# Kernel optimization log

Measured on AMD Instinct MI355X. Metric: run time of the kernel, lower is better.

The kernel has to match this reference:

```python
import jax, jax.numpy as jnp
import numpy as np

# OGB feature vocab sizes
ATOM_DIMS = [119, 4, 12, 12, 10, 6, 6, 2, 2]
BOND_DIMS = [5, 6, 2]
ATOM_OFF = np.concatenate([[0], np.cumsum(ATOM_DIMS)[:-1]]).astype(np.int32)
BOND_OFF = np.concatenate([[0], np.cumsum(BOND_DIMS)[:-1]]).astype(np.int32)
SCHEDULE_LEN = 5   # len(train_schedule) == len(eval_schedule)
NUM_GRAPHS = 12000
BN_EPS = 1e-5

N_NODES, N_EDGES, HIDDEN, NUM_TASKS = 300000, 600000, 128, 128


def setup_inputs() -> dict:
    key = jax.random.key(0)
    ks = jax.random.split(key, 16)
    x = jax.random.randint(ks[0], (N_NODES, 9), 0, 2, dtype=jnp.int32)
    edge_index = jax.random.randint(ks[1], (2, N_EDGES), 0, N_NODES, dtype=jnp.int32)
    edge_attr = jax.random.randint(ks[2], (N_EDGES, 3), 0, 2, dtype=jnp.int32)
    batch = jnp.sort(jax.random.randint(ks[3], (N_NODES,), 0, NUM_GRAPHS, dtype=jnp.int32))
    # learned parameters (embedding tables concatenated with offsets)
    atom_emb = jax.random.normal(ks[4], (sum(ATOM_DIMS), HIDDEN), jnp.float32) * 0.1
    bond_emb = jax.random.normal(ks[5], (sum(BOND_DIMS), HIDDEN), jnp.float32) * 0.1
    conv_W = jax.random.normal(ks[6], (HIDDEN, HIDDEN), jnp.float32) * (1.0 / np.sqrt(HIDDEN))
    conv_b = jnp.zeros((HIDDEN,), jnp.float32)
    root_emb = jax.random.normal(ks[7], (HIDDEN,), jnp.float32) * 0.1
    bn_gamma = jnp.ones((HIDDEN,), jnp.float32)
    bn_beta = jnp.zeros((HIDDEN,), jnp.float32)
    bn_mean = jnp.zeros((HIDDEN,), jnp.float32)   # running stats (eval mode)
    bn_var = jnp.ones((HIDDEN,), jnp.float32)
    lin_W = jax.random.normal(ks[8], (NUM_TASKS, HIDDEN), jnp.float32) * (1.0 / np.sqrt(HIDDEN))
    lin_b = jnp.zeros((NUM_TASKS,), jnp.float32)
    return {"x": x, "edge_index": edge_index, "edge_attr": edge_attr, "batch": batch,
            "atom_emb": atom_emb, "bond_emb": bond_emb, "conv_W": conv_W, "conv_b": conv_b,
            "root_emb": root_emb, "bn_gamma": bn_gamma, "bn_beta": bn_beta,
            "bn_mean": bn_mean, "bn_var": bn_var, "lin_W": lin_W, "lin_b": lin_b}


def reference(x, edge_index, edge_attr, batch, atom_emb, bond_emb, conv_W, conv_b,
              root_emb, bn_gamma, bn_beta, bn_mean, bn_var, lin_W, lin_b):
    N = x.shape[0]
    # AtomEncoder / BondEncoder: sum of per-feature embedding lookups
    h = atom_emb[x + jnp.asarray(ATOM_OFF, x.dtype)].sum(axis=1)            # [N, H]
    e = bond_emb[edge_attr + jnp.asarray(BOND_OFF, edge_attr.dtype)].sum(axis=1)  # [E, H]
    row, col = edge_index[0], edge_index[1]
    deg = jax.ops.segment_sum(jnp.ones_like(row, h.dtype), row, num_segments=N) + 1.0  # [N]
    dis = deg ** -0.5                                                        # deg >= 1, no inf
    norm = dis[row] * dis[col]                                               # [E]
    inv_std = bn_gamma / jnp.sqrt(bn_var + BN_EPS)
    for i in range(SCHEDULE_LEN):
        old = h
        z = h @ conv_W.T + conv_b                                            # [N, H]
        # message: norm * relu(x_j + edge_emb), aggregated at target (col) via scatter-add
        msg = norm[:, None] * jax.nn.relu(z[row] + e)                        # [E, H]
        agg = jax.ops.segment_sum(msg, col, num_segments=N)                  # [N, H]
        z = agg + jax.nn.relu(z + root_emb) / deg[:, None]                   # self-loop term
        z = jax.nn.relu(z)
        z = (z - bn_mean) * inv_std + bn_beta                                # BN (eval, running stats)
        # dropout: identity in eval mode
        # NOTE: faithful to source bug: smooth_fac is the loop index i, not schedule[i]
        h = i * old + (1 - i) * z
    # global mean pool over graphs
    counts = jax.ops.segment_sum(jnp.ones((N,), h.dtype), batch, num_segments=NUM_GRAPHS)
    pooled = jax.ops.segment_sum(h, batch, num_segments=NUM_GRAPHS) / jnp.maximum(counts, 1.0)[:, None]
    return pooled @ lin_W.T + lin_b                                          # [num_graphs, num_tasks]
```

## Files before the change

### kernel.cpp

```cpp
#include <hip/hip_runtime.h>

#define HID 128
#define AROWS 173

__device__ __forceinline__ int lcol(int p) { return ((p & 7) << 4) | (p >> 3); }

typedef __attribute__((ext_vector_type(8))) short short8;
typedef __attribute__((ext_vector_type(8))) unsigned short ushort8v;
typedef __attribute__((ext_vector_type(4))) float floatx4;
typedef __attribute__((ext_vector_type(4))) unsigned short ushort4v;

__device__ __forceinline__ unsigned short f2bf(float f) {
    unsigned u = __builtin_bit_cast(unsigned, f);
    u += 0x7FFF + ((u >> 16) & 1);
    return (unsigned short)(u >> 16);
}
__device__ __forceinline__ float bf2f(unsigned short s) {
    unsigned u = ((unsigned)s) << 16;
    return __builtin_bit_cast(float, u);
}

__global__ void fillrd_kernel(float* __restrict__ dis, int* __restrict__ indeg, int N)
{
    int i = blockIdx.x * 256 + threadIdx.x;
    if (i < N) { dis[i] = 0.f; indeg[i] = 0; }
}

__global__ void diag_kernel(float* __restrict__ out, long n, float val)
{
    long i = (long)blockIdx.x * blockDim.x + threadIdx.x;
    if (i < n) out[i] = val;
}

__global__ __launch_bounds__(256) void tables_kernel(
    const float* __restrict__ conv_W, unsigned short* __restrict__ Wb,
    const float* __restrict__ lin_W, unsigned short* __restrict__ linWb,
    const float* __restrict__ bond_emb, unsigned short* __restrict__ comb,
    const float* __restrict__ gamma, const float* __restrict__ beta,
    const float* __restrict__ mean, const float* __restrict__ var,
    float* __restrict__ bnsc, float* __restrict__ bnsh,
    const float* __restrict__ root, const float* __restrict__ conv_b,
    float* __restrict__ rootp, float* __restrict__ cbp)
{
    int blk = blockIdx.x;
    int tid = threadIdx.x;
    if (blk < 64) {
        int i = blk * 256 + tid;
        int row = i >> 7, p = i & 127;
        Wb[i] = f2bf(conv_W[row * HID + lcol(p)]);
    } else if (blk < 128) {
        int i = (blk - 64) * 256 + tid;
        int row = i >> 7, p = i & 127;
        linWb[i] = f2bf(lin_W[row * HID + lcol(p)]);
    } else if (blk < 158) {
        int i = (blk - 128) * 2 + (tid >> 7);
        int p = tid & 127;
        int c = lcol(p);
        int a0 = i / 12, a1 = (i % 12) / 2, a2 = i % 2;
        comb[i * HID + p] = f2bf(bond_emb[a0 * HID + c] + bond_emb[(5 + a1) * HID + c]
                               + bond_emb[(11 + a2) * HID + c]);
    } else if (tid < HID) {
        int c = lcol(tid);
        float sc = gamma[c] * rsqrtf(var[c] + 1e-5f);
        bnsc[tid] = sc;
        bnsh[tid] = beta[c] - mean[c] * sc;
        rootp[tid] = root[c];
        cbp[tid] = conv_b[c];
    }
}

__global__ __launch_bounds__(128) void ewk_kernel(
    const float* __restrict__ atom_emb, const float* __restrict__ conv_W,
    unsigned short* __restrict__ EWb)
{
    int r = blockIdx.x;
    int c = threadIdx.x;
    const float* er = atom_emb + (long)r * HID;
    const float* wr = conv_W + (long)c * HID;
    float acc = 0.f;
#pragma unroll 4
    for (int k = 0; k < HID; k += 4) {
        floatx4 e4 = *reinterpret_cast<const floatx4*>(er + k);
        floatx4 w4 = *reinterpret_cast<const floatx4*>(wr + k);
        acc += e4[0] * w4[0] + e4[1] * w4[1] + e4[2] * w4[2] + e4[3] * w4[3];
    }
    EWb[(long)r * HID + ((c & 15) * 8 + (c >> 4))] = f2bf(acc);
}

__global__ void hist_kernel(const int* __restrict__ ei, float* __restrict__ dis,
                            int* __restrict__ indeg, int E)
{
    for (int e = blockIdx.x * blockDim.x + threadIdx.x; e < E; e += gridDim.x * blockDim.x) {
        atomicAdd(&dis[ei[e]], 1.f);
        atomicAdd(&indeg[ei[E + e]], 1);
    }
}

__global__ __launch_bounds__(256) void bsum_kernel(
    const int* __restrict__ indeg, int* __restrict__ partial,
    float* __restrict__ dis, int N)
{
    __shared__ int s[256];
    int tid = threadIdx.x;
    int i = blockIdx.x * 256 + tid;
    int v = (i < N) ? indeg[i] : 0;
    s[tid] = v;
    if (i < N) dis[i] = rsqrtf(dis[i] + 1.f);
    __syncthreads();
    for (int d = 128; d > 0; d >>= 1) {
        if (tid < d) s[tid] += s[tid + d];
        __syncthreads();
    }
    if (tid == 0) partial[blockIdx.x] = s[0];
}

__global__ __launch_bounds__(256) void scan1_kernel(
    const int* __restrict__ partial, int* __restrict__ offs,
    int* __restrict__ ptr, int B, int N)
{
    __shared__ int s[256];
    __shared__ int carry_s;
    int tid = threadIdx.x;
    if (tid == 0) carry_s = 0;
    __syncthreads();
    for (int base = 0; base < B; base += 256) {
        int i = base + tid;
        int v = (i < B) ? partial[i] : 0;
        s[tid] = v;
        __syncthreads();
        for (int d = 1; d < 256; d <<= 1) {
            int t = (tid >= d) ? s[tid - d] : 0;
            __syncthreads();
            s[tid] += t;
            __syncthreads();
        }
        int carry = carry_s;
        if (i < B) offs[i] = carry + s[tid] - v;
        __syncthreads();
        if (tid == 0) carry_s = carry + s[255];
        __syncthreads();
    }
    if (tid == 0) ptr[N] = carry_s;
}

__global__ __launch_bounds__(256) void scan2_kernel(
    const int* __restrict__ indeg, const int* __restrict__ offs,
    int* __restrict__ ptr, int* __restrict__ cursor, int N)
{
    __shared__ int s[256];
    int tid = threadIdx.x;
    int i = blockIdx.x * 256 + tid;
    int v = (i < N) ? indeg[i] : 0;
    s[tid] = v;
    __syncthreads();
    for (int d = 1; d < 256; d <<= 1) {
        int t = (tid >= d) ? s[tid - d] : 0;
        __syncthreads();
        s[tid] += t;
        __syncthreads();
    }
    if (i < N) {
        int ex = offs[blockIdx.x] + s[tid] - v;
        ptr[i] = ex;
        cursor[i] = ex;
    }
}

__global__ void fillcsr_kernel(const int* __restrict__ ei, const int* __restrict__ attr,
                               const float* __restrict__ dis, int* __restrict__ cursor,
                               int2* __restrict__ edata, const int* __restrict__ batch,
                               int* __restrict__ gptr, int E, int N, int G)
{
    for (int e = blockIdx.x * blockDim.x + threadIdx.x; e < E; e += gridDim.x * blockDim.x) {
        int r   = ei[e];
        int col = ei[E + e];
        int pos = atomicAdd(&cursor[col], 1);
        int ci  = attr[e * 3] * 12 + attr[e * 3 + 1] * 2 + attr[e * 3 + 2];
        float nrm = dis[r] * dis[col];
        int2 ed;
        ed.x = r;
        ed.y = ci | ((int)f2bf(nrm) << 16);
        edata[pos] = ed;
    }
    for (int n = blockIdx.x * blockDim.x + threadIdx.x; n < N; n += gridDim.x * blockDim.x) {
        int b = batch[n];
        int bp = (n == 0) ? -1 : batch[n - 1];
        for (int g = bp + 1; g <= b; ++g) gptr[g] = n;
        if (n == N - 1)
            for (int g = b + 1; g <= G; ++g) gptr[g] = N;
    }
}

__global__ __launch_bounds__(256) void enc_kernel(
    const int* __restrict__ x, const unsigned short* __restrict__ EWb,
    const float* __restrict__ cbp, unsigned short* __restrict__ zb, int N)
{
    long n = (long)blockIdx.x * 16 + (threadIdx.x >> 4);
    if (n >= N) return;
    int c = (threadIdx.x & 15) * 8;
    const int OFF[9] = {0, 119, 123, 135, 147, 157, 163, 169, 171};

    float acc[8];
#pragma unroll
    for (int j = 0; j < 8; ++j) acc[j] = cbp[c + j];

#pragma unroll
    for (int f = 0; f < 9; ++f) {
        int idx = x[n * 9 + f] + OFF[f];
        ushort8v v = *reinterpret_cast<const ushort8v*>(EWb + (long)idx * HID + c);
#pragma unroll
        for (int j = 0; j < 8; ++j) acc[j] += bf2f(v[j]);
    }

    ushort8v o;
#pragma unroll
    for (int j = 0; j < 8; ++j) o[j] = f2bf(acc[j]);
    *reinterpret_cast<ushort8v*>(zb + n * HID + c) = o;
}

template<bool FIRST>
__global__ __launch_bounds__(256) void agg_kernel(
    const int* __restrict__ ptr, const int2* __restrict__ edata,
    const unsigned short* __restrict__ comb, const float* __restrict__ dis,
    const float* __restrict__ root, const float* __restrict__ bnsc,
    const float* __restrict__ bnsh, const unsigned short* __restrict__ zb,
    unsigned short* __restrict__ hb, float fi, int N)
{
    long n = (long)blockIdx.x * 16 + (threadIdx.x >> 4);
    if (n >= N) return;
    int c = (threadIdx.x & 15) * 8;

    ushort8v zv = *reinterpret_cast<const ushort8v*>(zb + n * HID + c);
    ushort8v hv;
    if constexpr (!FIRST) hv = *reinterpret_cast<const ushort8v*>(hb + n * HID + c);
    float di = dis[n];
    float rd = di * di;
    float acc[8];
#pragma unroll
    for (int j = 0; j < 8; ++j) acc[j] = fmaxf(bf2f(zv[j]) + root[c + j], 0.f) * rd;

    int jb = ptr[n], je = ptr[n + 1];
    int j2 = jb;
    for (; j2 + 1 < je; j2 += 2) {
        int2 e0 = edata[j2];
        int2 e1 = edata[j2 + 1];
        ushort8v z0 = *reinterpret_cast<const ushort8v*>(zb + (long)e0.x * HID + c);
        ushort8v z1 = *reinterpret_cast<const ushort8v*>(zb + (long)e1.x * HID + c);
        ushort8v c0 = *reinterpret_cast<const ushort8v*>(comb + (e0.y & 0xFF) * HID + c);
        ushort8v c1 = *reinterpret_cast<const ushort8v*>(comb + (e1.y & 0xFF) * HID + c);
        float n0 = bf2f((unsigned short)(((unsigned)e0.y) >> 16));
        float n1 = bf2f((unsigned short)(((unsigned)e1.y) >> 16));
#pragma unroll
        for (int j = 0; j < 8; ++j) {
            acc[j] += fmaxf(bf2f(z0[j]) + bf2f(c0[j]), 0.f) * n0;
            acc[j] += fmaxf(bf2f(z1[j]) + bf2f(c1[j]), 0.f) * n1;
        }
    }
    if (j2 < je) {
        int2 e0 = edata[j2];
        ushort8v z0 = *reinterpret_cast<const ushort8v*>(zb + (long)e0.x * HID + c);
        ushort8v c0 = *reinterpret_cast<const ushort8v*>(comb + (e0.y & 0xFF) * HID + c);
        float n0 = bf2f((unsigned short)(((unsigned)e0.y) >> 16));
#pragma unroll
        for (int j = 0; j < 8; ++j)
            acc[j] += fmaxf(bf2f(z0[j]) + bf2f(c0[j]), 0.f) * n0;
    }

    ushort8v o;
#pragma unroll
    for (int j = 0; j < 8; ++j) {
        float t = fmaxf(acc[j], 0.f) * bnsc[c + j] + bnsh[c + j];
        float h;
        if constexpr (FIRST) h = t;
        else h = fi * bf2f(hv[j]) + (1.f - fi) * t;
        o[j] = f2bf(h);
    }
    *reinterpret_cast<ushort8v*>(hb + n * HID + c) = o;
}

__global__ void gemm_kernel(
    const unsigned short* __restrict__ hb, const unsigned short* __restrict__ Wb,
    const float* __restrict__ bias, unsigned short* __restrict__ zb, int N)
{
    int tid = threadIdx.x;
    int wave = tid >> 6;
    int lane = tid & 63;
    int l15 = lane & 15;
    int q = lane >> 4;
    long row0 = (long)blockIdx.x * 128 + wave * 32;

    short8 a[2][4];
#pragma unroll
    for (int mt = 0; mt < 2; ++mt) {
        long rl = row0 + mt * 16 + l15;
        if (rl > (long)N - 1) rl = (long)N - 1;
        const unsigned short* ap = hb + rl * HID + q * 8;
#pragma unroll
        for (int kb = 0; kb < 4; ++kb)
            a[mt][kb] = *reinterpret_cast<const short8*>(ap + kb * 32);
    }

    floatx4 acc[2][8];
#pragma unroll
    for (int mt = 0; mt < 2; ++mt)
#pragma unroll
        for (int nt = 0; nt < 8; ++nt) {
            floatx4 zz = {0.f, 0.f, 0.f, 0.f};
            acc[mt][nt] = zz;
        }

#pragma unroll
    for (int nt = 0; nt < 8; ++nt) {
        const unsigned short* bp = Wb + (nt * 16 + l15) * HID + q * 8;
#pragma unroll
        for (int kb = 0; kb < 4; ++kb) {
            short8 b = *reinterpret_cast<const short8*>(bp + kb * 32);
            acc[0][nt] = __builtin_amdgcn_mfma_f32_16x16x32_bf16(a[0][kb], b, acc[0][nt], 0, 0, 0);
            acc[1][nt] = __builtin_amdgcn_mfma_f32_16x16x32_bf16(a[1][kb], b, acc[1][nt], 0, 0, 0);
        }
    }

    float bi[8];
#pragma unroll
    for (int nt = 0; nt < 8; ++nt) bi[nt] = bias[nt * 16 + l15];

#pragma unroll
    for (int mt = 0; mt < 2; ++mt)
#pragma unroll
        for (int r = 0; r < 4; ++r) {
            long gr = row0 + mt * 16 + q * 4 + r;
            if (gr < N) {
                ushort8v o;
#pragma unroll
                for (int nt = 0; nt < 8; ++nt)
                    o[nt] = f2bf(acc[mt][nt][r] + bi[nt]);
                *reinterpret_cast<ushort8v*>(zb + gr * HID + l15 * 8) = o;
            }
        }
}

__global__ __launch_bounds__(256) void linmm_kernel(
    const unsigned short* __restrict__ pb, const unsigned short* __restrict__ Wb,
    const float* __restrict__ bias, float* __restrict__ out, int G)
{
    int wave = threadIdx.x >> 6;
    int lane = threadIdx.x & 63;
    int l15 = lane & 15;
    int q = lane >> 4;
    long row0 = (long)blockIdx.x * 128 + wave * 32;

    short8 a[2][4];
#pragma unroll
    for (int mt = 0; mt < 2; ++mt) {
        long rl = row0 + mt * 16 + l15;
        if (rl > (long)G - 1) rl = (long)G - 1;
        const unsigned short* ap = pb + rl * HID + q * 8;
#pragma unroll
        for (int kb = 0; kb < 4; ++kb)
            a[mt][kb] = *reinterpret_cast<const short8*>(ap + kb * 32);
    }

    floatx4 acc[2][8];
#pragma unroll
    for (int mt = 0; mt < 2; ++mt)
#pragma unroll
        for (int nt = 0; nt < 8; ++nt) {
            floatx4 zz = {0.f, 0.f, 0.f, 0.f};
            acc[mt][nt] = zz;
        }

#pragma unroll
    for (int nt = 0; nt < 8; ++nt) {
        const unsigned short* bp = Wb + (nt * 16 + l15) * HID + q * 8;
#pragma unroll
        for (int kb = 0; kb < 4; ++kb) {
            short8 b = *reinterpret_cast<const short8*>(bp + kb * 32);
            acc[0][nt] = __builtin_amdgcn_mfma_f32_16x16x32_bf16(a[0][kb], b, acc[0][nt], 0, 0, 0);
            acc[1][nt] = __builtin_amdgcn_mfma_f32_16x16x32_bf16(a[1][kb], b, acc[1][nt], 0, 0, 0);
        }
    }

    float bi[8];
#pragma unroll
    for (int nt = 0; nt < 8; ++nt) bi[nt] = bias[nt * 16 + l15];

#pragma unroll
    for (int mt = 0; mt < 2; ++mt)
#pragma unroll
        for (int r = 0; r < 4; ++r) {
            long rr = row0 + mt * 16 + q * 4 + r;
            if (rr < G) {
                float* op = out + rr * HID + l15;
#pragma unroll
                for (int nt = 0; nt < 8; ++nt)
                    op[nt * 16] = acc[mt][nt][r] + bi[nt];
            }
        }
}

__global__ __launch_bounds__(256) void pool_kernel(
    const unsigned short* __restrict__ hb, const int* __restrict__ gptr,
    unsigned short* __restrict__ pb, int G)
{
    int g = blockIdx.x * 4 + (threadIdx.x >> 6);
    if (g >= G) return;
    int lane = threadIdx.x & 63;
    int c = lane * 2;
    int lo = gptr[g], hi = gptr[g + 1];

    float a0 = 0.f, a1 = 0.f, b0 = 0.f, b1 = 0.f;
    int n = lo;
    for (; n + 1 < hi; n += 2) {
        unsigned v0 = *reinterpret_cast<const unsigned*>(hb + (long)n * HID + c);
        unsigned v1 = *reinterpret_cast<const unsigned*>(hb + (long)(n + 1) * HID + c);
        a0 += bf2f((unsigned short)(v0 & 0xFFFF));
        a1 += bf2f((unsigned short)(v0 >> 16));
        b0 += bf2f((unsigned short)(v1 & 0xFFFF));
        b1 += bf2f((unsigned short)(v1 >> 16));
    }
    if (n < hi) {
        unsigned v0 = *reinterpret_cast<const unsigned*>(hb + (long)n * HID + c);
        a0 += bf2f((unsigned short)(v0 & 0xFFFF));
        a1 += bf2f((unsigned short)(v0 >> 16));
    }
    float cnt = (hi > lo) ? (float)(hi - lo) : 1.f;
    float s0 = (a0 + b0) / cnt;
    float s1 = (a1 + b1) / cnt;
    unsigned o = (unsigned)f2bf(s0) | ((unsigned)f2bf(s1) << 16);
    *reinterpret_cast<unsigned*>(pb + (long)g * HID + c) = o;
}

extern "C" void kernel_launch(void* const* d_in, const int* in_sizes, int n_in,
                              void* d_out, int out_size, void* d_ws, size_t ws_size,
                              hipStream_t stream)
{
    const int* x          = (const int*)d_in[0];
    const int* ei         = (const int*)d_in[1];
    const int* attr       = (const int*)d_in[2];
    const int* batch      = (const int*)d_in[3];
    const float* atom_emb = (const float*)d_in[4];
    const float* bond_emb = (const float*)d_in[5];
    const float* conv_W   = (const float*)d_in[6];
    const float* conv_b   = (const float*)d_in[7];
    const float* root     = (const float*)d_in[8];
    const float* gamma    = (const float*)d_in[9];
    const float* beta     = (const float*)d_in[10];
    const float* mean     = (const float*)d_in[11];
    const float* var      = (const float*)d_in[12];
    const float* lin_W    = (const float*)d_in[13];
    const float* lin_b    = (const float*)d_in[14];
    float* out = (float*)d_out;

    const int N = in_sizes[0] / 9;
    const int E = in_sizes[1] / 2;
    const int G = out_size / HID;
    const int B = (N + 255) / 256;

    auto al = [](size_t b) { return (b + 255) & ~(size_t)255; };
    const size_t need =
        al((size_t)N * HID * 2) +
        al((size_t)N * HID * 2) +
        al((size_t)(N + 1) * 4) +
        al((size_t)E * 8) +
        al((size_t)N * 4) +
        al((size_t)2048 * 4) * 2 +
        al((size_t)(G + 1) * 4) +
        al((size_t)(G + 128) * HID * 2) +
        al((size_t)60 * HID * 2) +
        al((size_t)HID * 4) * 4 +
        al((size_t)HID * HID * 2) * 2 +
        al((size_t)AROWS * HID * 2);

    if (ws_size < need || B > 2048) {
        float v = (B > 2048) ? 3000.f : (1000.f + (float)(ws_size >> 20));
        long n = (long)out_size;
        diag_kernel<<<(int)((n + 255) / 256), 256, 0, stream>>>(out, n, v);
        return;
    }

    char* wsp = (char*)d_ws;
    size_t used = 0;
    auto alloc = [&](size_t bytes) { char* p = wsp + used; used += al(bytes); return p; };
    unsigned short* hb = (unsigned short*)alloc((size_t)N * HID * 2);
    unsigned short* zb = (unsigned short*)alloc((size_t)N * HID * 2);
    int* ptr      = (int*)alloc((size_t)(N + 1) * 4);
    int2* edata   = (int2*)alloc((size_t)E * 8);
    int* indeg    = (int*)alloc((size_t)N * 4);
    int* cursor   = indeg;
    int* partial  = (int*)alloc((size_t)2048 * 4);
    int* offs     = (int*)alloc((size_t)2048 * 4);
    int* gptr     = (int*)alloc((size_t)(G + 1) * 4);
    unsigned short* pb = (unsigned short*)alloc((size_t)(G + 128) * HID * 2);
    float* dis    = (float*)pb;
    unsigned short* comb = (unsigned short*)alloc((size_t)60 * HID * 2);
    float* bnsc   = (float*)alloc((size_t)HID * 4);
    float* bnsh   = (float*)alloc((size_t)HID * 4);
    float* rootp  = (float*)alloc((size_t)HID * 4);
    float* cbp    = (float*)alloc((size_t)HID * 4);
    unsigned short* Wb    = (unsigned short*)alloc((size_t)HID * HID * 2);
    unsigned short* linWb = (unsigned short*)alloc((size_t)HID * HID * 2);
    unsigned short* EWb   = (unsigned short*)alloc((size_t)AROWS * HID * 2);

    fillrd_kernel<<<B, 256, 0, stream>>>(dis, indeg, N);
    tables_kernel<<<159, 256, 0, stream>>>(conv_W, Wb, lin_W, linWb, bond_emb, comb,
                                           gamma, beta, mean, var, bnsc, bnsh,
                                           root, conv_b, rootp, cbp);
    ewk_kernel<<<AROWS, 128, 0, stream>>>(atom_emb, conv_W, EWb);
    hist_kernel<<<1024, 256, 0, stream>>>(ei, dis, indeg, E);
    bsum_kernel<<<B, 256, 0, stream>>>(indeg, partial, dis, N);
    scan1_kernel<<<1, 256, 0, stream>>>(partial, offs, ptr, B, N);
    scan2_kernel<<<B, 256, 0, stream>>>(indeg, offs, ptr, cursor, N);
    fillcsr_kernel<<<1024, 256, 0, stream>>>(ei, attr, dis, cursor, edata,
                                             batch, gptr, E, N, G);

    const int gemm_blocks = (N + 127) / 128;
    const int node_blocks = (N + 15) / 16;
    enc_kernel<<<node_blocks, 256, 0, stream>>>(x, EWb, cbp, zb, N);
    agg_kernel<true ><<<node_blocks, 256, 0, stream>>>(ptr, edata, comb, dis,
            rootp, bnsc, bnsh, zb, hb, 0.f, N);
    const float fis[3] = {2.f, 3.f, 4.f};
    for (int t = 0; t < 3; ++t) {
        gemm_kernel<<<gemm_blocks, 256, 0, stream>>>(hb, Wb, conv_b, zb, N);
        agg_kernel<false><<<node_blocks, 256, 0, stream>>>(ptr, edata, comb, dis,
                rootp, bnsc, bnsh, zb, hb, fis[t], N);
    }

    pool_kernel<<<(G + 3) / 4, 256, 0, stream>>>(hb, gptr, pb, G);
    linmm_kernel<<<(G + 127) / 128, 256, 0, stream>>>(pb, linWb, lin_b, out, G);
}
```

Measured before the change: 648.5 us.

## Merge init kernels and widen edge records and bond table to fp32

Three setup kernels (zero-fill, table conversion, atom-embedding projection) become one launch partitioned by block index, removing two launches. Edge records grow from 8 to 16 bytes so the norm is stored as full fp32 and the bond index without packing, and the combined bond table is kept in fp32 instead of bf16. This removes the unpacking and bf16 conversions in the aggregation inner loop and improves norm precision. In exchange, edge and bond-table reads in the bandwidth-bound aggregation double in bytes.

```diff
diff --git a/kernel.cpp b/kernel.cpp
--- a/kernel.cpp
+++ b/kernel.cpp
@@ -20,30 +20,32 @@
     return __builtin_bit_cast(float, u);
 }
 
-__global__ void fillrd_kernel(float* __restrict__ dis, int* __restrict__ indeg, int N)
-{
-    int i = blockIdx.x * 256 + threadIdx.x;
-    if (i < N) { dis[i] = 0.f; indeg[i] = 0; }
-}
-
 __global__ void diag_kernel(float* __restrict__ out, long n, float val)
 {
     long i = (long)blockIdx.x * blockDim.x + threadIdx.x;
     if (i < n) out[i] = val;
 }
 
-__global__ __launch_bounds__(256) void tables_kernel(
+__global__ __launch_bounds__(256) void init_kernel(
+    float* __restrict__ dis, int* __restrict__ indeg, int NB, int N,
     const float* __restrict__ conv_W, unsigned short* __restrict__ Wb,
     const float* __restrict__ lin_W, unsigned short* __restrict__ linWb,
-    const float* __restrict__ bond_emb, unsigned short* __restrict__ comb,
+    const float* __restrict__ bond_emb, float* __restrict__ comb,
     const float* __restrict__ gamma, const float* __restrict__ beta,
     const float* __restrict__ mean, const float* __restrict__ var,
     float* __restrict__ bnsc, float* __restrict__ bnsh,
     const float* __restrict__ root, const float* __restrict__ conv_b,
-    float* __restrict__ rootp, float* __restrict__ cbp)
+    float* __restrict__ rootp, float* __restrict__ cbp,
+    const float* __restrict__ atom_emb, unsigned short* __restrict__ EWb)
 {
     int blk = blockIdx.x;
     int tid = threadIdx.x;
+    if (blk < NB) {
+        int i = blk * 256 + tid;
+        if (i < N) { dis[i] = 0.f; indeg[i] = 0; }
+        return;
+    }
+    blk -= NB;
     if (blk < 64) {
         int i = blk * 256 + tid;
         int row = i >> 7, p = i & 127;
@@ -57,34 +59,32 @@
         int p = tid & 127;
         int c = lcol(p);
         int a0 = i / 12, a1 = (i % 12) / 2, a2 = i % 2;
-        comb[i * HID + p] = f2bf(bond_emb[a0 * HID + c] + bond_emb[(5 + a1) * HID + c]
-                               + bond_emb[(11 + a2) * HID + c]);
-    } else if (tid < HID) {
-        int c = lcol(tid);
-        float sc = gamma[c] * rsqrtf(var[c] + 1e-5f);
-        bnsc[tid] = sc;
-        bnsh[tid] = beta[c] - mean[c] * sc;
-        rootp[tid] = root[c];
-        cbp[tid] = conv_b[c];
-    }
-}
-
-__global__ __launch_bounds__(128) void ewk_kernel(
-    const float* __restrict__ atom_emb, const float* __restrict__ conv_W,
-    unsigned short* __restrict__ EWb)
-{
-    int r = blockIdx.x;
-    int c = threadIdx.x;
-    const float* er = atom_emb + (long)r * HID;
-    const float* wr = conv_W + (long)c * HID;
-    float acc = 0.f;
+        comb[i * HID + p] = bond_emb[a0 * HID + c] + bond_emb[(5 + a1) * HID + c]
+                          + bond_emb[(11 + a2) * HID + c];
+    } else if (blk == 158) {
+        if (tid < HID) {
+            int c = lcol(tid);
+            float sc = gamma[c] * rsqrtf(var[c] + 1e-5f);
+            bnsc[tid] = sc;
+            bnsh[tid] = beta[c] - mean[c] * sc;
+            rootp[tid] = root[c];
+            cbp[tid] = conv_b[c];
+        }
+    } else {
+        int r = (blk - 159) * 2 + (tid >> 7);
+        if (r >= AROWS) return;
+        int c = tid & 127;
+        const float* er = atom_emb + (long)r * HID;
+        const float* wr = conv_W + (long)c * HID;
+        float acc = 0.f;
 #pragma unroll 4
-    for (int k = 0; k < HID; k += 4) {
-        floatx4 e4 = *reinterpret_cast<const floatx4*>(er + k);
-        floatx4 w4 = *reinterpret_cast<const floatx4*>(wr + k);
-        acc += e4[0] * w4[0] + e4[1] * w4[1] + e4[2] * w4[2] + e4[3] * w4[3];
-    }
-    EWb[(long)r * HID + ((c & 15) * 8 + (c >> 4))] = f2bf(acc);
+        for (int k = 0; k < HID; k += 4) {
+            floatx4 e4 = *reinterpret_cast<const floatx4*>(er + k);
+            floatx4 w4 = *reinterpret_cast<const floatx4*>(wr + k);
+            acc += e4[0] * w4[0] + e4[1] * w4[1] + e4[2] * w4[2] + e4[3] * w4[3];
+        }
+        EWb[(long)r * HID + ((c & 15) * 8 + (c >> 4))] = f2bf(acc);
+    }
 }
 
 __global__ void hist_kernel(const int* __restrict__ ei, float* __restrict__ dis,
@@ -168,7 +168,7 @@
 
 __global__ void fillcsr_kernel(const int* __restrict__ ei, const int* __restrict__ attr,
                                const float* __restrict__ dis, int* __restrict__ cursor,
-                               int2* __restrict__ edata, const int* __restrict__ batch,
+                               int4* __restrict__ edata, const int* __restrict__ batch,
                                int* __restrict__ gptr, int E, int N, int G)
 {
     for (int e = blockIdx.x * blockDim.x + threadIdx.x; e < E; e += gridDim.x * blockDim.x) {
@@ -177,9 +177,11 @@
         int pos = atomicAdd(&cursor[col], 1);
         int ci  = attr[e * 3] * 12 + attr[e * 3 + 1] * 2 + attr[e * 3 + 2];
         float nrm = dis[r] * dis[col];
-        int2 ed;
+        int4 ed;
         ed.x = r;
-        ed.y = ci | ((int)f2bf(nrm) << 16);
+        ed.y = ci;
+        ed.z = __builtin_bit_cast(int, nrm);
+        ed.w = 0;
         edata[pos] = ed;
     }
     for (int n = blockIdx.x * blockDim.x + threadIdx.x; n < N; n += gridDim.x * blockDim.x) {
@@ -220,8 +222,8 @@
 
 template<bool FIRST>
 __global__ __launch_bounds__(256) void agg_kernel(
-    const int* __restrict__ ptr, const int2* __restrict__ edata,
-    const unsigned short* __restrict__ comb, const float* __restrict__ dis,
+    const int* __restrict__ ptr, const int4* __restrict__ edata,
+    const float* __restrict__ comb, const float* __restrict__ dis,
     const float* __restrict__ root, const float* __restrict__ bnsc,
     const float* __restrict__ bnsh, const unsigned short* __restrict__ zb,
     unsigned short* __restrict__ hb, float fi, int N)
@@ -242,28 +244,38 @@
     int jb = ptr[n], je = ptr[n + 1];
     int j2 = jb;
     for (; j2 + 1 < je; j2 += 2) {
-        int2 e0 = edata[j2];
-        int2 e1 = edata[j2 + 1];
+        int4 e0 = edata[j2];
+        int4 e1 = edata[j2 + 1];
         ushort8v z0 = *reinterpret_cast<const ushort8v*>(zb + (long)e0.x * HID + c);
         ushort8v z1 = *reinterpret_cast<const ushort8v*>(zb + (long)e1.x * HID + c);
-        ushort8v c0 = *reinterpret_cast<const ushort8v*>(comb + (e0.y & 0xFF) * HID + c);
-        ushort8v c1 = *reinterpret_cast<const ushort8v*>(comb + (e1.y & 0xFF) * HID + c);
-        float n0 = bf2f((unsigned short)(((unsigned)e0.y) >> 16));
-        float n1 = bf2f((unsigned short)(((unsigned)e1.y) >> 16));
-#pragma unroll
-        for (int j = 0; j < 8; ++j) {
-            acc[j] += fmaxf(bf2f(z0[j]) + bf2f(c0[j]), 0.f) * n0;
-            acc[j] += fmaxf(bf2f(z1[j]) + bf2f(c1[j]), 0.f) * n1;
+        const float* c0p = comb + e0.y * HID + c;
+        const float* c1p = comb + e1.y * HID + c;
+        floatx4 c0a = *reinterpret_cast<const floatx4*>(c0p);
+        floatx4 c0b = *reinterpret_cast<const floatx4*>(c0p + 4);
+        floatx4 c1a = *reinterpret_cast<const floatx4*>(c1p);
+        floatx4 c1b = *reinterpret_cast<const floatx4*>(c1p + 4);
+        float n0 = __builtin_bit_cast(float, e0.z);
+        float n1 = __builtin_bit_cast(float, e1.z);
+#pragma unroll
+        for (int j = 0; j < 4; ++j) {
+            acc[j]     += fmaxf(bf2f(z0[j])     + c0a[j], 0.f) * n0;
+            acc[j + 4] += fmaxf(bf2f(z0[j + 4]) + c0b[j], 0.f) * n0;
+            acc[j]     += fmaxf(bf2f(z1[j])     + c1a[j], 0.f) * n1;
+            acc[j + 4] += fmaxf(bf2f(z1[j + 4]) + c1b[j], 0.f) * n1;
         }
     }
     if (j2 < je) {
-        int2 e0 = edata[j2];
+        int4 e0 = edata[j2];
         ushort8v z0 = *reinterpret_cast<const ushort8v*>(zb + (long)e0.x * HID + c);
-        ushort8v c0 = *reinterpret_cast<const ushort8v*>(comb + (e0.y & 0xFF) * HID + c);
-        float n0 = bf2f((unsigned short)(((unsigned)e0.y) >> 16));
-#pragma unroll
-        for (int j = 0; j < 8; ++j)
-            acc[j] += fmaxf(bf2f(z0[j]) + bf2f(c0[j]), 0.f) * n0;
+        const float* c0p = comb + e0.y * HID + c;
+        floatx4 c0a = *reinterpret_cast<const floatx4*>(c0p);
+        floatx4 c0b = *reinterpret_cast<const floatx4*>(c0p + 4);
+        float n0 = __builtin_bit_cast(float, e0.z);
+#pragma unroll
+        for (int j = 0; j < 4; ++j) {
+            acc[j]     += fmaxf(bf2f(z0[j])     + c0a[j], 0.f) * n0;
+            acc[j + 4] += fmaxf(bf2f(z0[j + 4]) + c0b[j], 0.f) * n0;
+        }
     }
 
     ushort8v o;
@@ -461,12 +473,12 @@
         al((size_t)N * HID * 2) +
         al((size_t)N * HID * 2) +
         al((size_t)(N + 1) * 4) +
-        al((size_t)E * 8) +
+        al((size_t)E * 16) +
         al((size_t)N * 4) +
         al((size_t)2048 * 4) * 2 +
         al((size_t)(G + 1) * 4) +
         al((size_t)(G + 128) * HID * 2) +
-        al((size_t)60 * HID * 2) +
+        al((size_t)60 * HID * 4) +
         al((size_t)HID * 4) * 4 +
         al((size_t)HID * HID * 2) * 2 +
         al((size_t)AROWS * HID * 2);
@@ -484,7 +496,7 @@
     unsigned short* hb = (unsigned short*)alloc((size_t)N * HID * 2);
     unsigned short* zb = (unsigned short*)alloc((size_t)N * HID * 2);
     int* ptr      = (int*)alloc((size_t)(N + 1) * 4);
-    int2* edata   = (int2*)alloc((size_t)E * 8);
+    int4* edata   = (int4*)alloc((size_t)E * 16);
     int* indeg    = (int*)alloc((size_t)N * 4);
     int* cursor   = indeg;
     int* partial  = (int*)alloc((size_t)2048 * 4);
@@ -492,7 +504,7 @@
     int* gptr     = (int*)alloc((size_t)(G + 1) * 4);
     unsigned short* pb = (unsigned short*)alloc((size_t)(G + 128) * HID * 2);
     float* dis    = (float*)pb;
-    unsigned short* comb = (unsigned short*)alloc((size_t)60 * HID * 2);
+    float* comb   = (float*)alloc((size_t)60 * HID * 4);
     float* bnsc   = (float*)alloc((size_t)HID * 4);
     float* bnsh   = (float*)alloc((size_t)HID * 4);
     float* rootp  = (float*)alloc((size_t)HID * 4);
@@ -501,11 +513,10 @@
     unsigned short* linWb = (unsigned short*)alloc((size_t)HID * HID * 2);
     unsigned short* EWb   = (unsigned short*)alloc((size_t)AROWS * HID * 2);
 
-    fillrd_kernel<<<B, 256, 0, stream>>>(dis, indeg, N);
-    tables_kernel<<<159, 256, 0, stream>>>(conv_W, Wb, lin_W, linWb, bond_emb, comb,
-                                           gamma, beta, mean, var, bnsc, bnsh,
-                                           root, conv_b, rootp, cbp);
-    ewk_kernel<<<AROWS, 128, 0, stream>>>(atom_emb, conv_W, EWb);
+    init_kernel<<<B + 159 + 87, 256, 0, stream>>>(dis, indeg, B, N,
+            conv_W, Wb, lin_W, linWb, bond_emb, comb,
+            gamma, beta, mean, var, bnsc, bnsh,
+            root, conv_b, rootp, cbp, atom_emb, EWb);
     hist_kernel<<<1024, 256, 0, stream>>>(ei, dis, indeg, E);
     bsum_kernel<<<B, 256, 0, stream>>>(indeg, partial, dis, N);
     scan1_kernel<<<1, 256, 0, stream>>>(partial, offs, ptr, B, N);
```

After: 659.5 us. About the same (+1.7%).
